# Kernel optimization log

Hardware: AMD Instinct MI355X
Metric: run time of the kernel (lower is better)

The kernel has to match this reference:

```python
import jax, jax.numpy as jnp
import numpy as np

H_IMG, W_IMG = 1024, 1280
MAX_ITER = 3
DAMPING = 1e-6
DIST_THR = 0.2
NORM_THR = float(np.cos(np.deg2rad(20.0)))


def setup_inputs() -> dict:
    key = jax.random.key(0)
    k1, k2, k3, k4 = jax.random.split(key, 4)
    H, W = H_IMG, W_IMG
    fx = fy = 1000.0
    cx, cy = (W - 1) / 2.0, (H - 1) / 2.0
    K = jnp.array([[fx, 0.0, cx], [0.0, fy, cy], [0.0, 0.0, 1.0]], dtype=jnp.float32)
    # backproject a random depth map so vertex maps are geometrically consistent with K
    depth = 0.5 + 2.5 * jax.random.uniform(k1, (H, W), dtype=jnp.float32)
    vv, uu = jnp.meshgrid(jnp.arange(H, dtype=jnp.float32), jnp.arange(W, dtype=jnp.float32), indexing='ij')
    vertex_t0 = jnp.stack([(uu - cx) / fx * depth, (vv - cy) / fy * depth, depth], axis=-1)
    n = jax.random.normal(k2, (H, W, 3), dtype=jnp.float32) * 0.1 + jnp.array([0.0, 0.0, -1.0], jnp.float32)
    normal_t0 = n / jnp.linalg.norm(n, axis=-1, keepdims=True)
    # frame 1 = slightly perturbed frame 0 (realistic small-motion ICP)
    vertex_t1 = vertex_t0 + 0.002 * jax.random.normal(k3, (H, W, 3), dtype=jnp.float32)
    n1 = normal_t0 + 0.01 * jax.random.normal(k4, (H, W, 3), dtype=jnp.float32)
    normal_t1 = n1 / jnp.linalg.norm(n1, axis=-1, keepdims=True)
    pose10 = jnp.eye(4, dtype=jnp.float32).at[:3, 3].set(jnp.array([0.005, -0.003, 0.002], jnp.float32))
    return {
        'pose10': pose10,
        'vertex_t0': vertex_t0.astype(jnp.float32),
        'vertex_t1': vertex_t1.astype(jnp.float32),
        'normal_t0': normal_t0.astype(jnp.float32),
        'normal_t1': normal_t1.astype(jnp.float32),
        'K': K,
    }


def _skew3(w):
    o = jnp.zeros((), w.dtype)
    return jnp.array([[o, -w[2], w[1]], [w[2], o, -w[0]], [-w[1], w[0], o]])


def _exp_se3(xi):
    w, v = xi[:3], xi[3:6]
    wh = _skew3(w)
    wh2 = wh @ wh
    theta = jnp.linalg.norm(w)
    eps = 1e-8
    ts = jnp.maximum(theta, eps)  # safe denominator
    sin_t, cos_t = jnp.sin(ts), jnp.cos(ts)
    eye3 = jnp.eye(3, dtype=xi.dtype)
    e_w_big = eye3 + wh * (sin_t / ts) + wh2 * ((1.0 - cos_t) / ts ** 2)
    j_big = eye3 + ((1.0 - cos_t) / ts ** 2) * wh + ((ts - sin_t) / ts ** 3) * wh2
    small = theta <= eps
    e_w = jnp.where(small, eye3, e_w_big)
    j = jnp.where(small, eye3, j_big)
    return jnp.eye(4, dtype=xi.dtype).at[:3, :3].set(e_w).at[:3, 3].set(j @ v)


def _warp_nearest(feat, u, v):
    # grid_sample(mode='nearest', padding='border', align_corners=True) with
    # the module's normalization reduces to nearest-pixel gather at (v,u), clamped.
    H, W, _ = feat.shape
    ui = jnp.clip(jnp.round(u), 0, W - 1).astype(jnp.int32)
    vi = jnp.clip(jnp.round(v), 0, H - 1).astype(jnp.int32)
    return feat[vi, ui]  # (H,W,C)


def _icp_step(pose, vertex0, vertex1, normal0, normal1, mask0, K):
    R, t = pose[:3, :3], pose[:3, 3]
    H, W, _ = vertex0.shape
    p = vertex0 @ R.T + t          # vertex0_to1, (H,W,3)
    n0 = normal0 @ R.T             # normal0_to1
    fx, fy, cx, cy = K[0, 0], K[1, 1], K[0, 2], K[1, 2]
    z = p[..., 2]
    u = p[..., 0] / z * fx + cx
    v = p[..., 1] / z * fy + cy
    inview = (u > 0) & (u < W - 1) & (v > 0) & (v < H - 1)
    rv1 = _warp_nearest(vertex1, u, v)
    rn1 = _warp_nearest(normal1, u, v)
    mask1 = rv1[..., -1] > 0.0
    diff = p - rv1
    normal_ok = jnp.sum(n0 * rn1, axis=-1) > NORM_THR
    res = jnp.sum(rn1 * diff, axis=-1)           # (H,W)
    # -n^T skew(p) == cross(p, n)
    J = jnp.concatenate([jnp.cross(p, rn1), rn1], axis=-1)  # (H,W,6)
    occ = (~inview) | (jnp.linalg.norm(diff, axis=-1) > DIST_THR)
    invalid = occ | (~mask0) | (~mask1) | (~normal_ok)
    J = jnp.where(invalid[..., None], 0.0, J).reshape(-1, 6)
    r = jnp.where(invalid, 0.0, res).reshape(-1)
    JtJ = J.T @ J                                 # (6,6)
    JtR = J.T @ r                                 # (6,)
    Hm = JtJ + jnp.trace(JtJ) * DAMPING * jnp.eye(6, dtype=JtJ.dtype)
    xi = -(jnp.linalg.inv(Hm) @ JtR)
    return _exp_se3(xi) @ pose, ~invalid


def reference(pose10, vertex_t0, vertex_t1, normal_t0, normal_t1, K):
    mask0 = vertex_t0[..., -1] > 0.0
    pose = pose10
    valid = None
    for _ in range(MAX_ITER):
        pose, valid = _icp_step(pose, vertex_t0, vertex_t1, normal_t0, normal_t1, mask0, K)
    H, W = vertex_t0.shape[:2]
    valid_ratio = valid.astype(jnp.float32).sum() / H / W
    return pose, valid_ratio
```

## Files before the change

### kernel.cpp

```cpp
#include <hip/hip_runtime.h>
#include <math.h>

#define H_IMG 1024
#define W_IMG 1280
#define NPIX (H_IMG * W_IMG)
#define NACC 28
#define NORM_THR 0.93969262f
#define DIST_THR2 0.04f
#define DAMPING 1e-6

__global__ __launch_bounds__(64) void icp_init(const float* __restrict__ pose_in,
                                               double* __restrict__ pose_ws) {
    int i = threadIdx.x;
    if (i < 16) pose_ws[i] = (double)pose_in[i];
}

__global__ __launch_bounds__(256) void icp_reduce(
    const float* __restrict__ vert0, const float* __restrict__ vert1,
    const float* __restrict__ norm0, const float* __restrict__ norm1,
    const float* __restrict__ Kmat,
    const double* __restrict__ pose_ws, double* __restrict__ acc)
{
    const float R00 = (float)pose_ws[0],  R01 = (float)pose_ws[1],  R02 = (float)pose_ws[2],  t0 = (float)pose_ws[3];
    const float R10 = (float)pose_ws[4],  R11 = (float)pose_ws[5],  R12 = (float)pose_ws[6],  t1 = (float)pose_ws[7];
    const float R20 = (float)pose_ws[8],  R21 = (float)pose_ws[9],  R22 = (float)pose_ws[10], t2 = (float)pose_ws[11];
    const float fx = Kmat[0], cx = Kmat[2], fy = Kmat[4], cy = Kmat[5];

    float a[NACC];
#pragma unroll
    for (int k = 0; k < NACC; ++k) a[k] = 0.0f;

    const int stride = gridDim.x * blockDim.x;
    for (int idx = blockIdx.x * blockDim.x + threadIdx.x; idx < NPIX; idx += stride) {
        const int base = idx * 3;
        const float v0x = vert0[base], v0y = vert0[base + 1], v0z = vert0[base + 2];
        const float n0x = norm0[base], n0y = norm0[base + 1], n0z = norm0[base + 2];

        const float px = R00 * v0x + R01 * v0y + R02 * v0z + t0;
        const float py = R10 * v0x + R11 * v0y + R12 * v0z + t1;
        const float pz = R20 * v0x + R21 * v0y + R22 * v0z + t2;
        const float nrx = R00 * n0x + R01 * n0y + R02 * n0z;
        const float nry = R10 * n0x + R11 * n0y + R12 * n0z;
        const float nrz = R20 * n0x + R21 * n0y + R22 * n0z;

        const float u = px / pz * fx + cx;
        const float v = py / pz * fy + cy;
        const bool inview = (u > 0.0f) && (u < (float)(W_IMG - 1)) &&
                            (v > 0.0f) && (v < (float)(H_IMG - 1));

        const float uf = fminf(fmaxf(rintf(u), 0.0f), (float)(W_IMG - 1));
        const float vf = fminf(fmaxf(rintf(v), 0.0f), (float)(H_IMG - 1));
        const int wbase = ((int)vf * W_IMG + (int)uf) * 3;

        const float r1x = vert1[wbase], r1y = vert1[wbase + 1], r1z = vert1[wbase + 2];
        const float m1x = norm1[wbase], m1y = norm1[wbase + 1], m1z = norm1[wbase + 2];

        const float dx = px - r1x, dy = py - r1y, dz = pz - r1z;

        const bool mask0 = v0z > 0.0f;
        const bool mask1 = r1z > 0.0f;
        const bool normal_ok = (nrx * m1x + nry * m1y + nrz * m1z) > NORM_THR;
        const float d2 = dx * dx + dy * dy + dz * dz;
        const bool occ = (!inview) || (d2 > DIST_THR2);
        const bool valid = (!occ) && mask0 && mask1 && normal_ok;

        if (valid) {
            const float res = m1x * dx + m1y * dy + m1z * dz;
            float J[6];
            J[0] = py * m1z - pz * m1y;
            J[1] = pz * m1x - px * m1z;
            J[2] = px * m1y - py * m1x;
            J[3] = m1x; J[4] = m1y; J[5] = m1z;
            int k = 0;
#pragma unroll
            for (int i = 0; i < 6; ++i)
#pragma unroll
                for (int j = i; j < 6; ++j) a[k++] += J[i] * J[j];
#pragma unroll
            for (int i = 0; i < 6; ++i) a[21 + i] += J[i] * res;
            a[27] += 1.0f;
        }
    }

#pragma unroll
    for (int k = 0; k < NACC; ++k) {
        float val = a[k];
        for (int off = 32; off > 0; off >>= 1) val += __shfl_down(val, off, 64);
        a[k] = val;
    }

    __shared__ float sh[4][NACC];
    const int lane = threadIdx.x & 63;
    const int wid  = threadIdx.x >> 6;
    if (lane == 0) {
#pragma unroll
        for (int k = 0; k < NACC; ++k) sh[wid][k] = a[k];
    }
    __syncthreads();
    if (threadIdx.x < NACC) {
        const int k = threadIdx.x;
        double s = (double)sh[0][k] + (double)sh[1][k] + (double)sh[2][k] + (double)sh[3][k];
        atomicAdd(&acc[k], s);
    }
}

__global__ __launch_bounds__(64) void icp_solve(const double* __restrict__ acc,
                                                double* __restrict__ pose_ws,
                                                float* __restrict__ out,
                                                int write_out)
{
    if (threadIdx.x != 0) return;

    double JtJ[6][6];
    {
        int k = 0;
        for (int i = 0; i < 6; ++i)
            for (int j = i; j < 6; ++j) { JtJ[i][j] = acc[k]; JtJ[j][i] = acc[k]; ++k; }
    }
    double JtR[6];
    for (int i = 0; i < 6; ++i) JtR[i] = acc[21 + i];

    double tr = 0.0;
    for (int i = 0; i < 6; ++i) tr += JtJ[i][i];

    double A[6][7];
    for (int i = 0; i < 6; ++i) {
        for (int j = 0; j < 6; ++j) A[i][j] = JtJ[i][j] + (i == j ? tr * DAMPING : 0.0);
        A[i][6] = -JtR[i];
    }

    for (int c = 0; c < 6; ++c) {
        int piv = c; double mx = fabs(A[c][c]);
        for (int r = c + 1; r < 6; ++r) {
            double ar = fabs(A[r][c]);
            if (ar > mx) { mx = ar; piv = r; }
        }
        if (piv != c) for (int j = 0; j < 7; ++j) { double tmp = A[c][j]; A[c][j] = A[piv][j]; A[piv][j] = tmp; }
        double d = A[c][c];
        if (d == 0.0) d = 1e-30;
        for (int r = c + 1; r < 6; ++r) {
            double f = A[r][c] / d;
            for (int j = c; j < 7; ++j) A[r][j] -= f * A[c][j];
        }
    }
    double xi[6];
    for (int i = 5; i >= 0; --i) {
        double s = A[i][6];
        for (int j = i + 1; j < 6; ++j) s -= A[i][j] * xi[j];
        double d = A[i][i];
        if (d == 0.0) d = 1e-30;
        xi[i] = s / d;
    }

    const double w0 = xi[0], w1 = xi[1], w2 = xi[2];
    const double v0 = xi[3], v1 = xi[4], v2 = xi[5];
    double wh[3][3] = { {0.0, -w2, w1}, {w2, 0.0, -w0}, {-w1, w0, 0.0} };
    double wh2[3][3];
    for (int i = 0; i < 3; ++i)
        for (int j = 0; j < 3; ++j) {
            double s = 0.0;
            for (int k = 0; k < 3; ++k) s += wh[i][k] * wh[k][j];
            wh2[i][j] = s;
        }
    const double theta = sqrt(w0 * w0 + w1 * w1 + w2 * w2);
    const double eps = 1e-8;
    const double ts = (theta > eps) ? theta : eps;
    const double st = sin(ts), ct = cos(ts);
    const double cA = st / ts;
    const double cB = (1.0 - ct) / (ts * ts);
    const double cC = (ts - st) / (ts * ts * ts);
    const bool small = (theta <= eps);

    double ew[3][3], Jm[3][3];
    for (int i = 0; i < 3; ++i)
        for (int j = 0; j < 3; ++j) {
            double eye = (i == j) ? 1.0 : 0.0;
            ew[i][j] = small ? eye : (eye + cA * wh[i][j] + cB * wh2[i][j]);
            Jm[i][j] = small ? eye : (eye + cB * wh[i][j] + cC * wh2[i][j]);
        }
    double Jv[3];
    for (int i = 0; i < 3; ++i) Jv[i] = Jm[i][0] * v0 + Jm[i][1] * v1 + Jm[i][2] * v2;

    double T[16] = { ew[0][0], ew[0][1], ew[0][2], Jv[0],
                     ew[1][0], ew[1][1], ew[1][2], Jv[1],
                     ew[2][0], ew[2][1], ew[2][2], Jv[2],
                     0.0, 0.0, 0.0, 1.0 };

    double P[16];
    for (int i = 0; i < 16; ++i) P[i] = pose_ws[i];
    double NP[16];
    for (int i = 0; i < 4; ++i)
        for (int j = 0; j < 4; ++j) {
            double s = 0.0;
            for (int k = 0; k < 4; ++k) s += T[i * 4 + k] * P[k * 4 + j];
            NP[i * 4 + j] = s;
        }
    for (int i = 0; i < 16; ++i) pose_ws[i] = NP[i];

    if (write_out) {
        for (int i = 0; i < 16; ++i) out[i] = (float)NP[i];
        out[16] = (float)(acc[27] / (double)NPIX);
    }
}

extern "C" void kernel_launch(void* const* d_in, const int* in_sizes, int n_in,
                              void* d_out, int out_size, void* d_ws, size_t ws_size,
                              hipStream_t stream) {
    const float* pose10 = (const float*)d_in[0];
    const float* vert0  = (const float*)d_in[1];
    const float* vert1  = (const float*)d_in[2];
    const float* norm0  = (const float*)d_in[3];
    const float* norm1  = (const float*)d_in[4];
    const float* Kmat   = (const float*)d_in[5];
    float* out = (float*)d_out;

    double* pose_ws = (double*)d_ws;
    double* acc     = pose_ws + 16;

    icp_init<<<1, 64, 0, stream>>>(pose10, pose_ws);
    for (int it = 0; it < 3; ++it) {
        hipMemsetAsync(acc, 0, NACC * sizeof(double), stream);
        icp_reduce<<<1024, 256, 0, stream>>>(vert0, vert1, norm0, norm1, Kmat, pose_ws, acc);
        icp_solve<<<1, 64, 0, stream>>>(acc, pose_ws, out, it == 2 ? 1 : 0);
    }
}
```

Measured before the change: 200.8 us.

## Fuse ICP reduce and solve via last-block pattern with vectorized loads

```diff
diff --git a/kernel.cpp b/kernel.cpp
--- a/kernel.cpp
+++ b/kernel.cpp
@@ -4,131 +4,42 @@
 #define H_IMG 1024
 #define W_IMG 1280
 #define NPIX (H_IMG * W_IMG)
+#define NQUAD (NPIX / 4)
+#define RBLOCKS 256
+#define RTPB 256
+#define QPT (NQUAD / (RBLOCKS * RTPB))
 #define NACC 28
+#define NREP 8
 #define NORM_THR 0.93969262f
 #define DIST_THR2 0.04f
 #define DAMPING 1e-6
 
-__global__ __launch_bounds__(64) void icp_init(const float* __restrict__ pose_in,
-                                               double* __restrict__ pose_ws) {
-    int i = threadIdx.x;
-    if (i < 16) pose_ws[i] = (double)pose_in[i];
-}
-
-__global__ __launch_bounds__(256) void icp_reduce(
-    const float* __restrict__ vert0, const float* __restrict__ vert1,
-    const float* __restrict__ norm0, const float* __restrict__ norm1,
-    const float* __restrict__ Kmat,
-    const double* __restrict__ pose_ws, double* __restrict__ acc)
-{
-    const float R00 = (float)pose_ws[0],  R01 = (float)pose_ws[1],  R02 = (float)pose_ws[2],  t0 = (float)pose_ws[3];
-    const float R10 = (float)pose_ws[4],  R11 = (float)pose_ws[5],  R12 = (float)pose_ws[6],  t1 = (float)pose_ws[7];
-    const float R20 = (float)pose_ws[8],  R21 = (float)pose_ws[9],  R22 = (float)pose_ws[10], t2 = (float)pose_ws[11];
-    const float fx = Kmat[0], cx = Kmat[2], fy = Kmat[4], cy = Kmat[5];
-
-    float a[NACC];
-#pragma unroll
-    for (int k = 0; k < NACC; ++k) a[k] = 0.0f;
-
-    const int stride = gridDim.x * blockDim.x;
-    for (int idx = blockIdx.x * blockDim.x + threadIdx.x; idx < NPIX; idx += stride) {
-        const int base = idx * 3;
-        const float v0x = vert0[base], v0y = vert0[base + 1], v0z = vert0[base + 2];
-        const float n0x = norm0[base], n0y = norm0[base + 1], n0z = norm0[base + 2];
-
-        const float px = R00 * v0x + R01 * v0y + R02 * v0z + t0;
-        const float py = R10 * v0x + R11 * v0y + R12 * v0z + t1;
-        const float pz = R20 * v0x + R21 * v0y + R22 * v0z + t2;
-        const float nrx = R00 * n0x + R01 * n0y + R02 * n0z;
-        const float nry = R10 * n0x + R11 * n0y + R12 * n0z;
-        const float nrz = R20 * n0x + R21 * n0y + R22 * n0z;
-
-        const float u = px / pz * fx + cx;
-        const float v = py / pz * fy + cy;
-        const bool inview = (u > 0.0f) && (u < (float)(W_IMG - 1)) &&
-                            (v > 0.0f) && (v < (float)(H_IMG - 1));
-
-        const float uf = fminf(fmaxf(rintf(u), 0.0f), (float)(W_IMG - 1));
-        const float vf = fminf(fmaxf(rintf(v), 0.0f), (float)(H_IMG - 1));
-        const int wbase = ((int)vf * W_IMG + (int)uf) * 3;
-
-        const float r1x = vert1[wbase], r1y = vert1[wbase + 1], r1z = vert1[wbase + 2];
-        const float m1x = norm1[wbase], m1y = norm1[wbase + 1], m1z = norm1[wbase + 2];
-
-        const float dx = px - r1x, dy = py - r1y, dz = pz - r1z;
-
-        const bool mask0 = v0z > 0.0f;
-        const bool mask1 = r1z > 0.0f;
-        const bool normal_ok = (nrx * m1x + nry * m1y + nrz * m1z) > NORM_THR;
-        const float d2 = dx * dx + dy * dy + dz * dz;
-        const bool occ = (!inview) || (d2 > DIST_THR2);
-        const bool valid = (!occ) && mask0 && mask1 && normal_ok;
-
-        if (valid) {
-            const float res = m1x * dx + m1y * dy + m1z * dz;
-            float J[6];
-            J[0] = py * m1z - pz * m1y;
-            J[1] = pz * m1x - px * m1z;
-            J[2] = px * m1y - py * m1x;
-            J[3] = m1x; J[4] = m1y; J[5] = m1z;
-            int k = 0;
-#pragma unroll
-            for (int i = 0; i < 6; ++i)
-#pragma unroll
-                for (int j = i; j < 6; ++j) a[k++] += J[i] * J[j];
-#pragma unroll
-            for (int i = 0; i < 6; ++i) a[21 + i] += J[i] * res;
-            a[27] += 1.0f;
-        }
-    }
-
-#pragma unroll
-    for (int k = 0; k < NACC; ++k) {
-        float val = a[k];
-        for (int off = 32; off > 0; off >>= 1) val += __shfl_down(val, off, 64);
-        a[k] = val;
-    }
-
-    __shared__ float sh[4][NACC];
-    const int lane = threadIdx.x & 63;
-    const int wid  = threadIdx.x >> 6;
-    if (lane == 0) {
-#pragma unroll
-        for (int k = 0; k < NACC; ++k) sh[wid][k] = a[k];
-    }
-    __syncthreads();
-    if (threadIdx.x < NACC) {
-        const int k = threadIdx.x;
-        double s = (double)sh[0][k] + (double)sh[1][k] + (double)sh[2][k] + (double)sh[3][k];
-        atomicAdd(&acc[k], s);
-    }
-}
-
-__global__ __launch_bounds__(64) void icp_solve(const double* __restrict__ acc,
-                                                double* __restrict__ pose_ws,
-                                                float* __restrict__ out,
-                                                int write_out)
-{
-    if (threadIdx.x != 0) return;
-
+#define ACC_DOUBLES (NREP * NACC * 8)
+
+__global__ __launch_bounds__(256) void icp_init(const float* __restrict__ pose_in,
+                                                double* __restrict__ ws) {
+    const int i = threadIdx.x;
+    if (i < 16) ws[i] = (double)pose_in[i];
+    for (int k = i; k < ACC_DOUBLES; k += 256) ws[16 + k] = 0.0;
+    if (i == 0) *(unsigned*)(ws + 16 + ACC_DOUBLES) = 0u;
+}
+
+__device__ void solve_and_update(const double* tot, double* pose_ws,
+                                 float* out, int write_out) {
     double JtJ[6][6];
     {
         int k = 0;
         for (int i = 0; i < 6; ++i)
-            for (int j = i; j < 6; ++j) { JtJ[i][j] = acc[k]; JtJ[j][i] = acc[k]; ++k; }
-    }
-    double JtR[6];
-    for (int i = 0; i < 6; ++i) JtR[i] = acc[21 + i];
-
+            for (int j = i; j < 6; ++j) { JtJ[i][j] = tot[k]; JtJ[j][i] = tot[k]; ++k; }
+    }
     double tr = 0.0;
     for (int i = 0; i < 6; ++i) tr += JtJ[i][i];
 
     double A[6][7];
     for (int i = 0; i < 6; ++i) {
         for (int j = 0; j < 6; ++j) A[i][j] = JtJ[i][j] + (i == j ? tr * DAMPING : 0.0);
-        A[i][6] = -JtR[i];
-    }
-
+        A[i][6] = -tot[21 + i];
+    }
     for (int c = 0; c < 6; ++c) {
         int piv = c; double mx = fabs(A[c][c]);
         for (int r = c + 1; r < 6; ++r) {
@@ -136,8 +47,7 @@
             if (ar > mx) { mx = ar; piv = r; }
         }
         if (piv != c) for (int j = 0; j < 7; ++j) { double tmp = A[c][j]; A[c][j] = A[piv][j]; A[piv][j] = tmp; }
-        double d = A[c][c];
-        if (d == 0.0) d = 1e-30;
+        double d = A[c][c]; if (d == 0.0) d = 1e-30;
         for (int r = c + 1; r < 6; ++r) {
             double f = A[r][c] / d;
             for (int j = c; j < 7; ++j) A[r][j] -= f * A[c][j];
@@ -147,8 +57,7 @@
     for (int i = 5; i >= 0; --i) {
         double s = A[i][6];
         for (int j = i + 1; j < 6; ++j) s -= A[i][j] * xi[j];
-        double d = A[i][i];
-        if (d == 0.0) d = 1e-30;
+        double d = A[i][i]; if (d == 0.0) d = 1e-30;
         xi[i] = s / d;
     }
 
@@ -185,7 +94,6 @@
                      ew[1][0], ew[1][1], ew[1][2], Jv[1],
                      ew[2][0], ew[2][1], ew[2][2], Jv[2],
                      0.0, 0.0, 0.0, 1.0 };
-
     double P[16];
     for (int i = 0; i < 16; ++i) P[i] = pose_ws[i];
     double NP[16];
@@ -199,7 +107,137 @@
 
     if (write_out) {
         for (int i = 0; i < 16; ++i) out[i] = (float)NP[i];
-        out[16] = (float)(acc[27] / (double)NPIX);
+        out[16] = (float)(tot[27] / (double)NPIX);
+    }
+}
+
+__global__ __launch_bounds__(RTPB) void icp_fused(
+    const float* __restrict__ vert0, const float* __restrict__ vert1,
+    const float* __restrict__ norm0, const float* __restrict__ norm1,
+    const float* __restrict__ Kmat, double* __restrict__ ws,
+    float* __restrict__ out, int write_out)
+{
+    const double* pose = ws;
+    double* acc = ws + 16;
+    unsigned* counter = (unsigned*)(ws + 16 + ACC_DOUBLES);
+
+    const float R00 = (float)pose[0],  R01 = (float)pose[1],  R02 = (float)pose[2],  t0 = (float)pose[3];
+    const float R10 = (float)pose[4],  R11 = (float)pose[5],  R12 = (float)pose[6],  t1 = (float)pose[7];
+    const float R20 = (float)pose[8],  R21 = (float)pose[9],  R22 = (float)pose[10], t2 = (float)pose[11];
+    const float fx = Kmat[0], cx = Kmat[2], fy = Kmat[4], cy = Kmat[5];
+
+    float a[NACC];
+#pragma unroll
+    for (int k = 0; k < NACC; ++k) a[k] = 0.0f;
+
+    auto do_pixel = [&](float v0x, float v0y, float v0z,
+                        float n0x, float n0y, float n0z) {
+        const float px = R00 * v0x + R01 * v0y + R02 * v0z + t0;
+        const float py = R10 * v0x + R11 * v0y + R12 * v0z + t1;
+        const float pz = R20 * v0x + R21 * v0y + R22 * v0z + t2;
+        const float nrx = R00 * n0x + R01 * n0y + R02 * n0z;
+        const float nry = R10 * n0x + R11 * n0y + R12 * n0z;
+        const float nrz = R20 * n0x + R21 * n0y + R22 * n0z;
+
+        const float u = px / pz * fx + cx;
+        const float v = py / pz * fy + cy;
+        const bool inview = (u > 0.0f) && (u < (float)(W_IMG - 1)) &&
+                            (v > 0.0f) && (v < (float)(H_IMG - 1));
+
+        const float uf = fminf(fmaxf(rintf(u), 0.0f), (float)(W_IMG - 1));
+        const float vf = fminf(fmaxf(rintf(v), 0.0f), (float)(H_IMG - 1));
+        const int wbase = ((int)vf * W_IMG + (int)uf) * 3;
+
+        const float r1x = vert1[wbase], r1y = vert1[wbase + 1], r1z = vert1[wbase + 2];
+        const float m1x = norm1[wbase], m1y = norm1[wbase + 1], m1z = norm1[wbase + 2];
+
+        const float dx = px - r1x, dy = py - r1y, dz = pz - r1z;
+        const bool mask0 = v0z > 0.0f;
+        const bool mask1 = r1z > 0.0f;
+        const bool normal_ok = (nrx * m1x + nry * m1y + nrz * m1z) > NORM_THR;
+        const float d2 = dx * dx + dy * dy + dz * dz;
+        const bool occ = (!inview) || (d2 > DIST_THR2);
+        const bool valid = (!occ) && mask0 && mask1 && normal_ok;
+
+        if (valid) {
+            const float res = m1x * dx + m1y * dy + m1z * dz;
+            float J[6];
+            J[0] = py * m1z - pz * m1y;
+            J[1] = pz * m1x - px * m1z;
+            J[2] = px * m1y - py * m1x;
+            J[3] = m1x; J[4] = m1y; J[5] = m1z;
+            int k = 0;
+#pragma unroll
+            for (int i = 0; i < 6; ++i)
+#pragma unroll
+                for (int j = i; j < 6; ++j) a[k++] += J[i] * J[j];
+#pragma unroll
+            for (int i = 0; i < 6; ++i) a[21 + i] += J[i] * res;
+            a[27] += 1.0f;
+        }
+    };
+
+    const int tid0 = blockIdx.x * RTPB + threadIdx.x;
+    const float4* v0q = (const float4*)vert0;
+    const float4* n0q = (const float4*)norm0;
+
+#pragma unroll
+    for (int i = 0; i < QPT; ++i) {
+        const int q = tid0 + i * (RBLOCKS * RTPB);
+        const float4 A0 = v0q[q * 3 + 0], A1 = v0q[q * 3 + 1], A2 = v0q[q * 3 + 2];
+        const float4 B0 = n0q[q * 3 + 0], B1 = n0q[q * 3 + 1], B2 = n0q[q * 3 + 2];
+        do_pixel(A0.x, A0.y, A0.z, B0.x, B0.y, B0.z);
+        do_pixel(A0.w, A1.x, A1.y, B0.w, B1.x, B1.y);
+        do_pixel(A1.z, A1.w, A2.x, B1.z, B1.w, B2.x);
+        do_pixel(A2.y, A2.z, A2.w, B2.y, B2.z, B2.w);
+    }
+
+#pragma unroll
+    for (int k = 0; k < NACC; ++k) {
+        float val = a[k];
+        for (int off = 32; off > 0; off >>= 1) val += __shfl_down(val, off, 64);
+        a[k] = val;
+    }
+
+    __shared__ float sh[4][NACC];
+    const int lane = threadIdx.x & 63;
+    const int wid  = threadIdx.x >> 6;
+    if (lane == 0) {
+#pragma unroll
+        for (int k = 0; k < NACC; ++k) sh[wid][k] = a[k];
+    }
+    __syncthreads();
+
+    const unsigned tid = threadIdx.x;
+    const int rep = blockIdx.x & (NREP - 1);
+    if (tid < NACC) {
+        double s = (double)sh[0][tid] + (double)sh[1][tid] +
+                   (double)sh[2][tid] + (double)sh[3][tid];
+        atomicAdd(&acc[(rep * NACC + (int)tid) * 8], s);
+        __threadfence();
+    }
+    __syncthreads();
+
+    __shared__ bool amLast;
+    if (tid == 0) {
+        unsigned prev = atomicAdd(counter, 1u);
+        amLast = (prev == gridDim.x - 1);
+    }
+    __syncthreads();
+
+    if (amLast) {
+        __shared__ double tot[NACC];
+        if (tid < NACC) {
+            double s = 0.0;
+            for (int r = 0; r < NREP; ++r)
+                s += atomicAdd(&acc[(r * NACC + (int)tid) * 8], 0.0);
+            tot[tid] = s;
+            for (int r = 0; r < NREP; ++r)
+                atomicExch((unsigned long long*)&acc[(r * NACC + (int)tid) * 8], 0ull);
+        }
+        if (tid == 0) atomicExch(counter, 0u);
+        __syncthreads();
+        if (tid == 0) solve_and_update(tot, ws, out, write_out);
     }
 }
 
@@ -213,14 +251,11 @@
     const float* norm1  = (const float*)d_in[4];
     const float* Kmat   = (const float*)d_in[5];
     float* out = (float*)d_out;
-
-    double* pose_ws = (double*)d_ws;
-    double* acc     = pose_ws + 16;
-
-    icp_init<<<1, 64, 0, stream>>>(pose10, pose_ws);
+    double* ws = (double*)d_ws;
+
+    icp_init<<<1, 256, 0, stream>>>(pose10, ws);
     for (int it = 0; it < 3; ++it) {
-        hipMemsetAsync(acc, 0, NACC * sizeof(double), stream);
-        icp_reduce<<<1024, 256, 0, stream>>>(vert0, vert1, norm0, norm1, Kmat, pose_ws, acc);
-        icp_solve<<<1, 64, 0, stream>>>(acc, pose_ws, out, it == 2 ? 1 : 0);
-    }
-}
+        icp_fused<<<RBLOCKS, RTPB, 0, stream>>>(vert0, vert1, norm0, norm1,
+                                                Kmat, ws, out, it == 2 ? 1 : 0);
+    }
+}
```

New measurement: 194.5 us. 1.03x faster.
